# Kernel tuning notes

Measured on AMD Instinct MI355X. Metric: run time of the kernel, lower is better.

## Reference

```python
import jax, jax.numpy as jnp
import numpy as np

N, C_IN, C_OUT, C_REL, T, V = 64, 256, 256, 32, 64, 25

def conv1x1(x, w, b):
    # x: (n, ci, a, b), w: (co, ci), b: (co,) -> (n, co, a, b)
    return jnp.einsum('oc,ncab->noab', w, x) + b[None, :, None, None]

def setup_inputs() -> dict:
    key = jax.random.key(0)
    ks = jax.random.split(key, 10)
    s_in = 1.0 / np.sqrt(C_IN)
    s_rel = 1.0 / np.sqrt(C_REL)
    return {
        'x': jax.random.normal(ks[0], (N, C_IN, T, V), dtype=jnp.float32),
        'A': jax.random.normal(ks[1], (V, V), dtype=jnp.float32),
        'w1': jax.random.uniform(ks[2], (C_REL, C_IN), jnp.float32, -s_in, s_in),
        'b1': jax.random.uniform(ks[3], (C_REL,), jnp.float32, -s_in, s_in),
        'w2': jax.random.uniform(ks[4], (C_REL, C_IN), jnp.float32, -s_in, s_in),
        'b2': jax.random.uniform(ks[5], (C_REL,), jnp.float32, -s_in, s_in),
        'w3': jax.random.uniform(ks[6], (C_OUT, C_IN), jnp.float32, -s_in, s_in),
        'b3': jax.random.uniform(ks[7], (C_OUT,), jnp.float32, -s_in, s_in),
        'w4': jax.random.uniform(ks[8], (C_OUT, C_REL), jnp.float32, -s_rel, s_rel),
        'b4': jax.random.uniform(ks[9], (C_OUT,), jnp.float32, -s_rel, s_rel),
        'threhold': 0,
        'alpha': 1,
    }

def reference(x, A, w1, b1, w2, b2, w3, b3, w4, b4, threhold, alpha):
    # x: (n, c, t, v)
    # pooled 1x1 convs: fold the T-mean before the channel mix (linear ops commute)
    xm = x.mean(-2)                                   # (n, c, v)
    x1 = jnp.einsum('oc,ncv->nov', w1, xm) + b1[None, :, None]   # (n, r, v)
    x2 = jnp.einsum('oc,ncv->nov', w2, xm) + b2[None, :, None]   # (n, r, v)
    x3 = conv1x1(x, w3, b3)                           # (n, co, t, v)
    # channel-wise affinity: outer difference + tanh -> (n, r, v, v)
    aff = jnp.tanh(x1[:, :, :, None] - x2[:, :, None, :])
    # 1x1 conv over rel channels, scale, add adjacency
    attn = jnp.einsum('or,nruv->nouv', w4, aff) + b4[None, :, None, None]
    attn = attn * alpha + A[None, None]               # (n, co, v, v)
    # graph conv contraction
    out = jnp.einsum('ncuv,nctu->nctv', attn, x3)     # (n, co, t, v)
    return out
```

## Files before the change

### kernel.cpp

```cpp
#include <hip/hip_runtime.h>

#define N_  64
#define CI  256
#define CO  256
#define CR  32
#define T_  64
#define V_  25
#define TV  (T_*V_)
#define VV  (V_*V_)
#define ATS 640

typedef __attribute__((ext_vector_type(8))) short bshort8;
typedef __attribute__((ext_vector_type(4))) float f32x4;

__device__ inline unsigned short f2bf(float f) {
    unsigned int u = __float_as_uint(f);
    return (unsigned short)((u + 0x7FFFu + ((u >> 16) & 1u)) >> 16);
}

__global__ __launch_bounds__(256) void k_cvt_w(const float* __restrict__ w3,
                                               const float* __restrict__ w4,
                                               unsigned short* __restrict__ w3f,
                                               unsigned short* __restrict__ w4f) {
    int b = blockIdx.x;
    if (b < 32) {
        int f = b * 256 + threadIdx.x;
        int lane = f & 63;
        int ks = (f >> 6) & 7;
        int ot = f >> 9;
        const float* src = w3 + (size_t)(ot * 16 + (lane & 15)) * CI + ks * 32 + (lane >> 4) * 8;
        bshort8 v;
        #pragma unroll
        for (int i = 0; i < 8; ++i) v[i] = (short)f2bf(src[i]);
        *(bshort8*)(w3f + (size_t)f * 8) = v;
    } else {
        int f = (b - 32) * 256 + threadIdx.x;
        int lane = f & 63;
        int ot = f >> 6;
        const float* src = w4 + (size_t)(ot * 16 + (lane & 15)) * CR + (lane >> 4) * 8;
        bshort8 v;
        #pragma unroll
        for (int i = 0; i < 8; ++i) v[i] = (short)f2bf(src[i]);
        *(bshort8*)(w4f + (size_t)f * 8) = v;
    }
}

__global__ __launch_bounds__(256) void k_mean(const float* __restrict__ x,
                                              float* __restrict__ xm) {
    int idx = blockIdx.x * 256 + threadIdx.x;
    if (idx >= N_ * CI * V_) return;
    int v  = idx % V_;
    int nc = idx / V_;
    const float* p = x + (size_t)nc * TV + v;
    float s = 0.f;
    for (int t = 0; t < T_; ++t) s += p[t * V_];
    xm[idx] = s * (1.f / T_);
}

__global__ __launch_bounds__(256) void k_x1x2(const float* __restrict__ xm,
                                              const float* __restrict__ w1,
                                              const float* __restrict__ b1,
                                              const float* __restrict__ w2,
                                              const float* __restrict__ b2,
                                              float* __restrict__ x1,
                                              float* __restrict__ x2) {
    int n = blockIdx.x;
    __shared__ float s_xm[CI * V_];
    const float4* src = (const float4*)(xm + (size_t)n * CI * V_);
    for (int i = threadIdx.x; i < CI * V_ / 4; i += 256) ((float4*)s_xm)[i] = src[i];
    __syncthreads();
    for (int idx = threadIdx.x; idx < CR * V_; idx += 256) {
        int r = idx / V_, v = idx % V_;
        float a1 = 0.f, a2 = 0.f;
        for (int c = 0; c < CI; ++c) {
            float xv = s_xm[c * V_ + v];
            a1 += w1[r * CI + c] * xv;
            a2 += w2[r * CI + c] * xv;
        }
        x1[n * CR * V_ + idx] = a1 + b1[r];
        x2[n * CR * V_ + idx] = a2 + b2[r];
    }
}

__global__ __launch_bounds__(256) void k_attn(const float* __restrict__ x1,
                                              const float* __restrict__ x2,
                                              const unsigned short* __restrict__ w4f,
                                              const float* __restrict__ b4,
                                              const float* __restrict__ A,
                                              const int* __restrict__ alpha_p,
                                              unsigned short* __restrict__ attnT) {
    int n = blockIdx.x;
    __shared__ float s_x1[CR * V_];
    __shared__ float s_x2[CR * V_];
    __shared__ float s_A[VV];
    int tid = threadIdx.x;
    float alpha = (float)alpha_p[0];
    for (int i = tid; i < CR * V_; i += 256) {
        s_x1[i] = x1[n * CR * V_ + i];
        s_x2[i] = x2[n * CR * V_ + i];
    }
    for (int i = tid; i < VV; i += 256) s_A[i] = A[i];
    __syncthreads();
    int wave = tid >> 6, lane = tid & 63;
    int task = blockIdx.y * 4 + wave;
    int og   = task & 3;
    int ug   = task >> 2;
    int o0   = og * 64;
    int quad = lane >> 4, c16 = lane & 15;
    bshort8 a[4];
    #pragma unroll
    for (int ot = 0; ot < 4; ++ot)
        a[ot] = *(const bshort8*)(w4f + (size_t)(((og * 4) + ot) * 64 + lane) * 8);
    float4 bv[4];
    #pragma unroll
    for (int ot = 0; ot < 4; ++ot)
        bv[ot] = *(const float4*)(b4 + o0 + ot * 16 + quad * 4);
    int r0 = quad * 8;
    #pragma unroll
    for (int it = 0; it < 5; ++it) {
        int uv0 = (ug * 5 + it) * 16;
        int uvc = uv0 + c16;
        bool valid = uvc < VV;
        int uvcc = valid ? uvc : (VV - 1);
        int u = uvcc % V_, v = uvcc / V_;
        bshort8 b;
        #pragma unroll
        for (int i = 0; i < 8; ++i) {
            float d = s_x1[(r0 + i) * V_ + u] - s_x2[(r0 + i) * V_ + v];
            b[i] = (short)f2bf(tanhf(d));
        }
        float Auv = s_A[u * V_ + v];
        f32x4 acc[4];
        #pragma unroll
        for (int ot = 0; ot < 4; ++ot)
            acc[ot] = __builtin_amdgcn_mfma_f32_16x16x32_bf16(a[ot], b, (f32x4){0,0,0,0}, 0, 0, 0);
        if (valid) {
            #pragma unroll
            for (int ot = 0; ot < 4; ++ot) {
                #pragma unroll
                for (int r = 0; r < 4; ++r) {
                    int o = o0 + ot * 16 + quad * 4 + r;
                    float bval = (r == 0) ? bv[ot].x : (r == 1) ? bv[ot].y
                               : (r == 2) ? bv[ot].z : bv[ot].w;
                    attnT[(size_t)(n * CO + o) * ATS + uvc] =
                        f2bf((acc[ot][r] + bval) * alpha + Auv);
                }
            }
        }
    }
}

__global__ __launch_bounds__(256) void k_gemm1(const float* __restrict__ x,
                                               const unsigned short* __restrict__ w3f,
                                               const float* __restrict__ b3,
                                               unsigned short* __restrict__ x3) {
    int n = blockIdx.x, j0 = blockIdx.y * 64;
    __shared__ unsigned short sB[64 * 256];
    int tid  = threadIdx.x;
    int lane = tid & 63, wave = tid >> 6;
    const float* gx = x + (size_t)n * CI * TV + j0;
    for (int i = 0; i < 16; ++i) {
        int task = i * 256 + tid;
        int c = task >> 4, chunk = task & 15;
        float4 v = *(const float4*)(gx + (size_t)c * TV + chunk * 4);
        int g0 = c >> 3, cl = c & 7;
        #pragma unroll
        for (int k = 0; k < 4; ++k) {
            int j = chunk * 4 + k;
            int f = g0 ^ (j & 7) ^ ((j >> 2) & 7);
            float val = (k == 0) ? v.x : (k == 1) ? v.y : (k == 2) ? v.z : v.w;
            sB[j * 256 + f * 8 + cl] = f2bf(val);
        }
    }
    __syncthreads();
    int quad = lane >> 4, c16 = lane & 15;
    const bshort8* Af = (const bshort8*)w3f;
    f32x4 acc[4][4];
    #pragma unroll
    for (int mt = 0; mt < 4; ++mt)
        #pragma unroll
        for (int nt = 0; nt < 4; ++nt) acc[mt][nt] = (f32x4){0,0,0,0};
    #pragma unroll
    for (int ks = 0; ks < 8; ++ks) {
        bshort8 b[4], a[4];
        #pragma unroll
        for (int nt = 0; nt < 4; ++nt) {
            int rB = nt * 16 + c16;
            int cidx = ks * 4 + quad;
            int f = cidx ^ (rB & 7) ^ ((rB >> 2) & 7);
            b[nt] = *(const bshort8*)(&sB[rB * 256 + f * 8]);
        }
        #pragma unroll
        for (int mt = 0; mt < 4; ++mt)
            a[mt] = Af[(size_t)(((wave * 4 + mt) * 8 + ks) * 64) + lane];
        #pragma unroll
        for (int mt = 0; mt < 4; ++mt)
            #pragma unroll
            for (int nt = 0; nt < 4; ++nt)
                acc[mt][nt] = __builtin_amdgcn_mfma_f32_16x16x32_bf16(a[mt], b[nt], acc[mt][nt], 0, 0, 0);
    }
    __syncthreads();
    unsigned short* eS = sB;
    #pragma unroll
    for (int pass = 0; pass < 2; ++pass) {
        if ((wave >> 1) == pass) {
            #pragma unroll
            for (int mt = 0; mt < 4; ++mt) {
                int o = wave * 64 + mt * 16 + quad * 4;
                float4 bvv = *(const float4*)(b3 + o);
                int ol = (wave & 1) * 64 + mt * 16 + quad * 4;
                #pragma unroll
                for (int nt = 0; nt < 4; ++nt) {
                    int jc = nt * 16 + c16;
                    eS[(ol + 0) * 72 + jc] = f2bf(acc[mt][nt][0] + bvv.x);
                    eS[(ol + 1) * 72 + jc] = f2bf(acc[mt][nt][1] + bvv.y);
                    eS[(ol + 2) * 72 + jc] = f2bf(acc[mt][nt][2] + bvv.z);
                    eS[(ol + 3) * 72 + jc] = f2bf(acc[mt][nt][3] + bvv.w);
                }
            }
        }
        __syncthreads();
        #pragma unroll
        for (int i = 0; i < 4; ++i) {
            int task = i * 256 + tid;
            int orow = task >> 3, seg = task & 7;
            bshort8 vv = *(const bshort8*)&eS[orow * 72 + seg * 8];
            *(bshort8*)(x3 + (size_t)(n * CO + pass * 128 + orow) * TV + j0 + seg * 8) = vv;
        }
        __syncthreads();
    }
}

__global__ __launch_bounds__(256) void k_contract(const unsigned short* __restrict__ x3,
                                                  const unsigned short* __restrict__ attnT,
                                                  float* __restrict__ out) {
    int no0 = blockIdx.x * 4;
    __shared__ __align__(16) unsigned char smem[28672];
    unsigned short* sA = (unsigned short*)smem;
    unsigned short* sB = (unsigned short*)(smem + 16384);
    float*          sO = (float*)smem;
    int tid = threadIdx.x;
    #pragma unroll
    for (int i = 0; i < 7; ++i) {
        int task = i * 256 + tid;
        if (task < 1792) {
            int p = task / 448, rem = task % 448;
            sA[p * 2048 + (rem / 7) * 32 + 25 + rem % 7] = 0;
        }
    }
    {
        int task = tid;
        for (int i = 0; i < 3; ++i, task += 256)
            if (task < 700) {
                int p = task / 175, rem = task % 175;
                sB[p * 1024 + (rem / 7) * 32 + 25 + rem % 7] = 0;
            }
    }
    #pragma unroll
    for (int i = 0; i < 4; ++i) {
        int task = i * 256 + tid;
        if (task < 800) {
            int p = task / 200, e8 = task % 200;
            bshort8 vv = *(const bshort8*)(x3 + (size_t)(no0 + p) * TV + e8 * 8);
            #pragma unroll
            for (int k = 0; k < 8; ++k) {
                int j = e8 * 8 + k;
                int t = j / 25, u = j % 25;
                sA[p * 2048 + t * 32 + u] = (unsigned short)vv[k];
            }
        }
    }
    #pragma unroll
    for (int i = 0; i < 2; ++i) {
        int task = i * 256 + tid;
        if (task < 316) {
            int p = task / 79, e8 = task % 79;
            bshort8 vv = *(const bshort8*)(attnT + (size_t)(no0 + p) * ATS + e8 * 8);
            #pragma unroll
            for (int k = 0; k < 8; ++k) {
                int idx = e8 * 8 + k;
                if (idx < VV) {
                    int v = idx / 25, u = idx % 25;
                    sB[p * 1024 + v * 32 + u] = (unsigned short)vv[k];
                }
            }
        }
    }
    __syncthreads();
    int p = tid >> 6, lane = tid & 63;
    int quad = lane >> 4, c16 = lane & 15;
    const unsigned short* pA = sA + p * 2048;
    const unsigned short* pB = sB + p * 1024;
    bshort8 a[4], b[2];
    #pragma unroll
    for (int mt = 0; mt < 4; ++mt) a[mt] = *(const bshort8*)&pA[(mt * 16 + c16) * 32 + quad * 8];
    #pragma unroll
    for (int nt = 0; nt < 2; ++nt) b[nt] = *(const bshort8*)&pB[(nt * 16 + c16) * 32 + quad * 8];
    f32x4 acc[4][2];
    #pragma unroll
    for (int mt = 0; mt < 4; ++mt)
        #pragma unroll
        for (int nt = 0; nt < 2; ++nt)
            acc[mt][nt] = __builtin_amdgcn_mfma_f32_16x16x32_bf16(a[mt], b[nt], (f32x4){0,0,0,0}, 0, 0, 0);
    __syncthreads();
    float* pO = sO + p * 1792;
    #pragma unroll
    for (int mt = 0; mt < 4; ++mt)
        #pragma unroll
        for (int nt = 0; nt < 2; ++nt) {
            int v = nt * 16 + c16;
            if (v < V_) {
                #pragma unroll
                for (int r = 0; r < 4; ++r) {
                    int t = mt * 16 + quad * 4 + r;
                    pO[t * 28 + v] = acc[mt][nt][r];
                }
            }
        }
    __syncthreads();
    #pragma unroll
    for (int i = 0; i < 25; ++i) {
        int idx = i * 256 + tid;
        int p2 = idx / TV, rem = idx % TV;
        int t = rem / 25, v = rem % 25;
        out[(size_t)(no0 + p2) * TV + rem] = sO[p2 * 1792 + t * 28 + v];
    }
}

extern "C" void kernel_launch(void* const* d_in, const int* in_sizes, int n_in,
                              void* d_out, int out_size, void* d_ws, size_t ws_size,
                              hipStream_t stream) {
    const float* x  = (const float*)d_in[0];
    const float* A  = (const float*)d_in[1];
    const float* w1 = (const float*)d_in[2];
    const float* b1 = (const float*)d_in[3];
    const float* w2 = (const float*)d_in[4];
    const float* b2 = (const float*)d_in[5];
    const float* w3 = (const float*)d_in[6];
    const float* b3 = (const float*)d_in[7];
    const float* w4 = (const float*)d_in[8];
    const float* b4 = (const float*)d_in[9];
    const int* alpha_p = (const int*)d_in[11];
    float* out = (float*)d_out;

    float* ws = (float*)d_ws;
    float* xm = ws;
    float* x1 = ws + 409600;
    float* x2 = ws + 460800;
    unsigned short* attnT = (unsigned short*)(ws + 512000);
    unsigned short* w3f   = attnT + (size_t)16384 * ATS;
    unsigned short* w4f   = w3f + 65536;
    unsigned short* x3    = w4f + 16384;

    k_cvt_w<<<36, 256, 0, stream>>>(w3, w4, w3f, w4f);
    k_mean<<<(N_ * CI * V_ + 255) / 256, 256, 0, stream>>>(x, xm);
    k_x1x2<<<N_, 256, 0, stream>>>(xm, w1, b1, w2, b2, x1, x2);
    k_attn<<<dim3(N_, 8), 256, 0, stream>>>(x1, x2, w4f, b4, A, alpha_p, attnT);
    k_gemm1<<<dim3(N_, 25), 256, 0, stream>>>(x, w3f, b3, x3);
    k_contract<<<4096, 256, 0, stream>>>(x3, attnT, out);
}
```

Baseline: 323.2 us.

## Fuse mean/weight-convert and x1x2 into attn kernel, store attn in MFMA-ready layout

Merges the T-mean and w3 conversion into one launch, folds the x1/x2 projection and the w4 bf16 conversion into the attention kernel, and drops three launches and their intermediate buffers. The attention output is now written in a padded 32x32 per-channel layout with zeroed padding, so the contraction kernel loads its B fragments straight from global memory and skips the LDS staging pass. In exchange, each attention block recomputes x1/x2 for its batch (8x redundant across blockIdx.y), and the attention buffer grows from 640 to 1024 entries per row.

Result: slower. 363.9 us (+12.6%).

```diff
diff --git a/kernel.cpp b/kernel.cpp
--- a/kernel.cpp
+++ b/kernel.cpp
@@ -8,7 +8,7 @@
 #define V_  25
 #define TV  (T_*V_)
 #define VV  (V_*V_)
-#define ATS 640
+#define ATS2 1024
 
 typedef __attribute__((ext_vector_type(8))) short bshort8;
 typedef __attribute__((ext_vector_type(4))) float f32x4;
@@ -18,13 +18,21 @@
     return (unsigned short)((u + 0x7FFFu + ((u >> 16) & 1u)) >> 16);
 }
 
-__global__ __launch_bounds__(256) void k_cvt_w(const float* __restrict__ w3,
-                                               const float* __restrict__ w4,
-                                               unsigned short* __restrict__ w3f,
-                                               unsigned short* __restrict__ w4f) {
+__global__ __launch_bounds__(256) void k_mean_cvt(const float* __restrict__ x,
+                                                  const float* __restrict__ w3,
+                                                  float* __restrict__ xm,
+                                                  unsigned short* __restrict__ w3f) {
     int b = blockIdx.x;
-    if (b < 32) {
-        int f = b * 256 + threadIdx.x;
+    if (b < 1600) {
+        int idx = b * 256 + threadIdx.x;
+        int v  = idx % V_;
+        int nc = idx / V_;
+        const float* p = x + (size_t)nc * TV + v;
+        float s = 0.f;
+        for (int t = 0; t < T_; ++t) s += p[t * V_];
+        xm[idx] = s * (1.f / T_);
+    } else {
+        int f = (b - 1600) * 256 + threadIdx.x;
         int lane = f & 63;
         int ks = (f >> 6) & 7;
         int ot = f >> 9;
@@ -33,84 +41,62 @@
         #pragma unroll
         for (int i = 0; i < 8; ++i) v[i] = (short)f2bf(src[i]);
         *(bshort8*)(w3f + (size_t)f * 8) = v;
-    } else {
-        int f = (b - 32) * 256 + threadIdx.x;
-        int lane = f & 63;
-        int ot = f >> 6;
-        const float* src = w4 + (size_t)(ot * 16 + (lane & 15)) * CR + (lane >> 4) * 8;
-        bshort8 v;
-        #pragma unroll
-        for (int i = 0; i < 8; ++i) v[i] = (short)f2bf(src[i]);
-        *(bshort8*)(w4f + (size_t)f * 8) = v;
-    }
-}
-
-__global__ __launch_bounds__(256) void k_mean(const float* __restrict__ x,
-                                              float* __restrict__ xm) {
-    int idx = blockIdx.x * 256 + threadIdx.x;
-    if (idx >= N_ * CI * V_) return;
-    int v  = idx % V_;
-    int nc = idx / V_;
-    const float* p = x + (size_t)nc * TV + v;
-    float s = 0.f;
-    for (int t = 0; t < T_; ++t) s += p[t * V_];
-    xm[idx] = s * (1.f / T_);
-}
-
-__global__ __launch_bounds__(256) void k_x1x2(const float* __restrict__ xm,
+    }
+}
+
+__global__ __launch_bounds__(256) void k_attn(const float* __restrict__ xm,
                                               const float* __restrict__ w1,
                                               const float* __restrict__ b1,
                                               const float* __restrict__ w2,
                                               const float* __restrict__ b2,
-                                              float* __restrict__ x1,
-                                              float* __restrict__ x2) {
-    int n = blockIdx.x;
-    __shared__ float s_xm[CI * V_];
-    const float4* src = (const float4*)(xm + (size_t)n * CI * V_);
-    for (int i = threadIdx.x; i < CI * V_ / 4; i += 256) ((float4*)s_xm)[i] = src[i];
-    __syncthreads();
-    for (int idx = threadIdx.x; idx < CR * V_; idx += 256) {
-        int r = idx / V_, v = idx % V_;
-        float a1 = 0.f, a2 = 0.f;
-        for (int c = 0; c < CI; ++c) {
-            float xv = s_xm[c * V_ + v];
-            a1 += w1[r * CI + c] * xv;
-            a2 += w2[r * CI + c] * xv;
-        }
-        x1[n * CR * V_ + idx] = a1 + b1[r];
-        x2[n * CR * V_ + idx] = a2 + b2[r];
-    }
-}
-
-__global__ __launch_bounds__(256) void k_attn(const float* __restrict__ x1,
-                                              const float* __restrict__ x2,
-                                              const unsigned short* __restrict__ w4f,
+                                              const float* __restrict__ w4,
                                               const float* __restrict__ b4,
                                               const float* __restrict__ A,
                                               const int* __restrict__ alpha_p,
                                               unsigned short* __restrict__ attnT) {
-    int n = blockIdx.x;
+    int n  = blockIdx.x;
+    int by = blockIdx.y;
     __shared__ float s_x1[CR * V_];
     __shared__ float s_x2[CR * V_];
     __shared__ float s_A[VV];
     int tid = threadIdx.x;
     float alpha = (float)alpha_p[0];
-    for (int i = tid; i < CR * V_; i += 256) {
-        s_x1[i] = x1[n * CR * V_ + i];
-        s_x2[i] = x2[n * CR * V_ + i];
+    const float* xmn = xm + (size_t)n * CI * V_;
+    for (int idx = tid; idx < CR * V_; idx += 256) {
+        int r = idx / V_, v = idx % V_;
+        const float* wr1 = w1 + (size_t)r * CI;
+        const float* wr2 = w2 + (size_t)r * CI;
+        float p1a = 0.f, p1b = 0.f, p2a = 0.f, p2b = 0.f;
+        #pragma unroll 4
+        for (int c = 0; c < CI; c += 2) {
+            float xv0 = xmn[c * V_ + v];
+            float xv1 = xmn[(c + 1) * V_ + v];
+            p1a += wr1[c] * xv0;  p1b += wr1[c + 1] * xv1;
+            p2a += wr2[c] * xv0;  p2b += wr2[c + 1] * xv1;
+        }
+        s_x1[idx] = p1a + p1b + b1[r];
+        s_x2[idx] = p2a + p2b + b2[r];
     }
     for (int i = tid; i < VV; i += 256) s_A[i] = A[i];
     __syncthreads();
     int wave = tid >> 6, lane = tid & 63;
-    int task = blockIdx.y * 4 + wave;
-    int og   = task & 3;
-    int ug   = task >> 2;
-    int o0   = og * 64;
+    int og = wave;
+    int ug = by;
+    int o0 = og * 64;
     int quad = lane >> 4, c16 = lane & 15;
     bshort8 a[4];
     #pragma unroll
-    for (int ot = 0; ot < 4; ++ot)
-        a[ot] = *(const bshort8*)(w4f + (size_t)(((og * 4) + ot) * 64 + lane) * 8);
+    for (int ot = 0; ot < 4; ++ot) {
+        const float* src = w4 + (size_t)((og * 4 + ot) * 16 + c16) * CR + quad * 8;
+        float4 v0 = *(const float4*)src;
+        float4 v1 = *(const float4*)(src + 4);
+        bshort8 t;
+        t[0] = (short)f2bf(v0.x); t[1] = (short)f2bf(v0.y);
+        t[2] = (short)f2bf(v0.z); t[3] = (short)f2bf(v0.w);
+        t[4] = (short)f2bf(v1.x); t[5] = (short)f2bf(v1.y);
+        t[6] = (short)f2bf(v1.z); t[7] = (short)f2bf(v1.w);
+        a[ot] = t;
+    }
     float4 bv[4];
     #pragma unroll
     for (int ot = 0; ot < 4; ++ot)
@@ -142,11 +128,19 @@
                     int o = o0 + ot * 16 + quad * 4 + r;
                     float bval = (r == 0) ? bv[ot].x : (r == 1) ? bv[ot].y
                                : (r == 2) ? bv[ot].z : bv[ot].w;
-                    attnT[(size_t)(n * CO + o) * ATS + uvc] =
+                    attnT[(size_t)(n * CO + o) * ATS2 + v * 32 + u] =
                         f2bf((acc[ot][r] + bval) * alpha + Auv);
                 }
             }
         }
+    }
+    int vlo = (by * 25) >> 3;
+    int nv  = (((by + 1) * 25) >> 3) - vlo;
+    for (int i = tid; i < 256 * nv; i += 256) {
+        int o = i / nv, v = vlo + i % nv;
+        unsigned short* pp = attnT + (size_t)(n * CO + o) * ATS2 + v * 32 + 25;
+        #pragma unroll
+        for (int u = 0; u < 7; ++u) pp[u] = 0;
     }
 }
 
@@ -237,7 +231,6 @@
     int no0 = blockIdx.x * 4;
     __shared__ __align__(16) unsigned char smem[28672];
     unsigned short* sA = (unsigned short*)smem;
-    unsigned short* sB = (unsigned short*)(smem + 16384);
     float*          sO = (float*)smem;
     int tid = threadIdx.x;
     #pragma unroll
@@ -247,14 +240,6 @@
             int p = task / 448, rem = task % 448;
             sA[p * 2048 + (rem / 7) * 32 + 25 + rem % 7] = 0;
         }
-    }
-    {
-        int task = tid;
-        for (int i = 0; i < 3; ++i, task += 256)
-            if (task < 700) {
-                int p = task / 175, rem = task % 175;
-                sB[p * 1024 + (rem / 7) * 32 + 25 + rem % 7] = 0;
-            }
     }
     #pragma unroll
     for (int i = 0; i < 4; ++i) {
@@ -270,32 +255,17 @@
             }
         }
     }
-    #pragma unroll
-    for (int i = 0; i < 2; ++i) {
-        int task = i * 256 + tid;
-        if (task < 316) {
-            int p = task / 79, e8 = task % 79;
-            bshort8 vv = *(const bshort8*)(attnT + (size_t)(no0 + p) * ATS + e8 * 8);
-            #pragma unroll
-            for (int k = 0; k < 8; ++k) {
-                int idx = e8 * 8 + k;
-                if (idx < VV) {
-                    int v = idx / 25, u = idx % 25;
-                    sB[p * 1024 + v * 32 + u] = (unsigned short)vv[k];
-                }
-            }
-        }
-    }
     __syncthreads();
     int p = tid >> 6, lane = tid & 63;
     int quad = lane >> 4, c16 = lane & 15;
     const unsigned short* pA = sA + p * 2048;
-    const unsigned short* pB = sB + p * 1024;
+    const unsigned short* pBg = attnT + (size_t)(no0 + p) * ATS2;
     bshort8 a[4], b[2];
     #pragma unroll
     for (int mt = 0; mt < 4; ++mt) a[mt] = *(const bshort8*)&pA[(mt * 16 + c16) * 32 + quad * 8];
     #pragma unroll
-    for (int nt = 0; nt < 2; ++nt) b[nt] = *(const bshort8*)&pB[(nt * 16 + c16) * 32 + quad * 8];
+    for (int nt = 0; nt < 2; ++nt)
+        b[nt] = *(const bshort8*)(pBg + (size_t)(nt * 16 + c16) * 32 + quad * 8);
     f32x4 acc[4][2];
     #pragma unroll
     for (int mt = 0; mt < 4; ++mt)
@@ -345,17 +315,12 @@
 
     float* ws = (float*)d_ws;
     float* xm = ws;
-    float* x1 = ws + 409600;
-    float* x2 = ws + 460800;
-    unsigned short* attnT = (unsigned short*)(ws + 512000);
-    unsigned short* w3f   = attnT + (size_t)16384 * ATS;
-    unsigned short* w4f   = w3f + 65536;
-    unsigned short* x3    = w4f + 16384;
-
-    k_cvt_w<<<36, 256, 0, stream>>>(w3, w4, w3f, w4f);
-    k_mean<<<(N_ * CI * V_ + 255) / 256, 256, 0, stream>>>(x, xm);
-    k_x1x2<<<N_, 256, 0, stream>>>(xm, w1, b1, w2, b2, x1, x2);
-    k_attn<<<dim3(N_, 8), 256, 0, stream>>>(x1, x2, w4f, b4, A, alpha_p, attnT);
+    unsigned short* attnT = (unsigned short*)(ws + 409600);
+    unsigned short* w3f   = attnT + (size_t)16384 * ATS2;
+    unsigned short* x3    = w3f + 65536;
+
+    k_mean_cvt<<<1632, 256, 0, stream>>>(x, w3, xm, w3f);
+    k_attn<<<dim3(N_, 8), 256, 0, stream>>>(xm, w1, b1, w2, b2, w4, b4, A, alpha_p, attnT);
     k_gemm1<<<dim3(N_, 25), 256, 0, stream>>>(x, w3f, b3, x3);
     k_contract<<<4096, 256, 0, stream>>>(x3, attnT, out);
 }
```
